# Performance work log

Hardware: AMD Instinct MI355X
Metric: run time of the kernel (lower is better)

Reference implementation:

```python
import jax, jax.numpy as jnp
import numpy as np

H_OUT = 8
W_OUT = 8
MAXG = 4  # max adaptive sampling grid per bin: ceil((H-1)/H_OUT) with H=32


def _flip_table():
    h, w = H_OUT, W_OUT
    ys = np.repeat(np.arange(h), w)
    xs = np.tile(np.arange(w), h)
    rys = np.repeat(np.arange(h - 1, -1, -1), w)
    # NOTE: original torch code does arange(w-1,-1,-1).reshape(h,1).repeat(1,w)
    # which makes reverse_xs a per-ROW reversal (requires h==w); replicated faithfully.
    rxs = np.repeat(np.arange(w - 1, -1, -1), w)
    i00 = ys * w + xs
    i01 = ys * w + rxs
    i10 = rys * w + xs
    i11 = rys * w + rxs
    # original stacks [i00, i01, i01, i10, i11]; idx_idxs in {0..3} so entry for
    # (y_rev=1,x_rev=0) is i01 (duplicated) and (1,1) hits i10; i11 is unused. Replicated.
    return jnp.asarray(np.stack([i00, i01, i01, i10, i11]), dtype=jnp.int32)

_TABLE = _flip_table()


def _axis_samples(start, bin_sz, grid, n_out, size):
    # start, bin_sz: [N] float; grid: [N] int (adaptive samples per bin along this axis)
    # returns low/high neighbor indices and corner weights, each [N, n_out*MAXG]
    N = start.shape[0]
    g_safe = jnp.maximum(grid, 1).astype(start.dtype)
    ph = jnp.arange(n_out, dtype=start.dtype)
    i = jnp.arange(MAXG, dtype=start.dtype)
    pos = (start[:, None, None]
           + ph[None, :, None] * bin_sz[:, None, None]
           + (i[None, None, :] + 0.5) * (bin_sz / g_safe)[:, None, None])  # [N,n_out,MAXG]
    valid = ((pos >= -1.0) & (pos <= size)
             & (jnp.arange(MAXG)[None, None, :] < grid[:, None, None]))
    p = jnp.clip(pos, 0.0, size - 1)
    low = jnp.floor(p).astype(jnp.int32)
    high = jnp.minimum(low + 1, size - 1)
    l = p - low.astype(p.dtype)
    vf = valid.astype(start.dtype)
    return (low.reshape(N, -1), high.reshape(N, -1),
            ((1.0 - l) * vf).reshape(N, -1), (l * vf).reshape(N, -1))


def _roi_align_flip(feats, batch_idxs, starts, goals):
    B, C, H, W = feats.shape
    N = starts.shape[0]
    s = starts.astype(feats.dtype)
    g = goals.astype(feats.dtype)
    y_min = jnp.minimum(s[:, 0], g[:, 0]); y_max = jnp.maximum(s[:, 0], g[:, 0])
    x_min = jnp.minimum(s[:, 1], g[:, 1]); x_max = jnp.maximum(s[:, 1], g[:, 1])
    y_rev = s[:, 0] > g[:, 0]
    x_rev = s[:, 1] > g[:, 1]
    # torchvision roi_align: aligned=True, spatial_scale=1.0, sampling_ratio=-1
    start_h = y_min - 0.5; start_w = x_min - 0.5
    roi_h = y_max - y_min; roi_w = x_max - x_min
    bin_h = roi_h / H_OUT; bin_w = roi_w / W_OUT
    gh = jnp.ceil(bin_h).astype(jnp.int32)
    gw = jnp.ceil(bin_w).astype(jnp.int32)
    count = jnp.maximum(gh * gw, 1).astype(feats.dtype)
    ylo, yhi, wy0, wy1 = _axis_samples(start_h, bin_h, gh, H_OUT, H)  # [N, H_OUT*MAXG]
    xlo, xhi, wx0, wx1 = _axis_samples(start_w, bin_w, gw, W_OUT, W)  # [N, W_OUT*MAXG]
    fv = feats.reshape(B, C, H * W)[batch_idxs]  # [N,C,H*W] per-box feature slab
    hM, wM = H_OUT * MAXG, W_OUT * MAXG

    def gath(yi, xi):
        lin = (yi[:, :, None] * W + xi[:, None, :]).reshape(N, 1, hM * wM)
        v = jnp.take_along_axis(fv, jnp.broadcast_to(lin, (N, C, hM * wM)), axis=2)
        return v.reshape(N, C, hM, wM)

    def outer(a, b):
        return a[:, None, :, None] * b[:, None, None, :]

    acc = (gath(ylo, xlo) * outer(wy0, wx0)
           + gath(ylo, xhi) * outer(wy0, wx1)
           + gath(yhi, xlo) * outer(wy1, wx0)
           + gath(yhi, xhi) * outer(wy1, wx1))  # [N,C,hM,wM]
    rois = acc.reshape(N, C, H_OUT, MAXG, W_OUT, MAXG).sum(axis=(3, 5))
    rois = rois / count[:, None, None, None]
    # per-box orientation flip via index-table gather
    idx_idxs = y_rev.astype(jnp.int32) * 2 + x_rev.astype(jnp.int32)
    sel = _TABLE[idx_idxs]  # [N, h*w]
    rflat = rois.reshape(N, C, H_OUT * W_OUT)
    out = jnp.take_along_axis(rflat, jnp.broadcast_to(sel[:, None, :], rflat.shape), axis=2)
    return out.reshape(N, C, H_OUT, W_OUT)


def setup_inputs() -> dict:
    key = jax.random.key(0)
    k1, k2, k3, k4 = jax.random.split(key, 4)
    B, C, H, W = 8, 64, 32, 32
    N = 1024  # B * A with A = 128 agents
    feats = jax.random.normal(k1, (B, C, H, W), dtype=jnp.float32)
    batch_idxs = jax.random.randint(k2, (N,), 0, B, dtype=jnp.int32)
    starts = jax.random.randint(k3, (N, 2), 0, H, dtype=jnp.int32)
    goals = jax.random.randint(k4, (N, 2), 0, H, dtype=jnp.int32)
    return {"feats": feats, "batch_idxs": batch_idxs, "starts": starts, "goals": goals}


def reference(feats, batch_idxs, starts, goals):
    return _roi_align_flip(feats, batch_idxs, starts, goals)
```

## Files before the change

### kernel.cpp

```cpp
#include <hip/hip_runtime.h>

#define H_OUT 8
#define W_OUT 8
#define MAXG 4
#define CCHUNK 8
#define RSLOTS 6

__global__ __launch_bounds__(256) void ordered_roi_kernel(
    const float* __restrict__ feats,
    const int*   __restrict__ batch_idxs,
    const int*   __restrict__ starts,
    const int*   __restrict__ goals,
    float*       __restrict__ out,
    int C, int CG)
{
    const int bx  = blockIdx.x;
    const int n   = bx / CG;
    const int cg  = bx - n * CG;
    const int tid = threadIdx.x;

    const float s0 = (float)starts[2 * n + 0];
    const float s1 = (float)starts[2 * n + 1];
    const float g0 = (float)goals[2 * n + 0];
    const float g1 = (float)goals[2 * n + 1];
    const float y_min = fminf(s0, g0), y_max = fmaxf(s0, g0);
    const float x_min = fminf(s1, g1), x_max = fmaxf(s1, g1);
    const bool  y_rev = s0 > g0;
    const bool  x_rev = s1 > g1;
    const float start_h = y_min - 0.5f;
    const float start_w = x_min - 0.5f;
    const float bin_h = (y_max - y_min) / (float)H_OUT;
    const float bin_w = (x_max - x_min) / (float)W_OUT;
    const int   gh = (int)ceilf(bin_h);
    const int   gw = (int)ceilf(bin_w);
    const float inv_count = 1.0f / fmaxf((float)(gh * gw), 1.0f);

    __shared__ int   s_rbase[2][H_OUT];
    __shared__ int   s_rcnt[2][H_OUT];
    __shared__ float s_rw[2][H_OUT][RSLOTS];
    __shared__ float s_t[CCHUNK][H_OUT][33];

    if (tid < 16) {
        const int axis = tid >> 3;
        const int ph   = tid & 7;
        const float start = axis ? start_w : start_h;
        const float bin   = axis ? bin_w  : bin_h;
        const int   grid  = axis ? gw     : gh;
        const float gsafe = (float)(grid > 1 ? grid : 1);
        float wloc[RSLOTS] = {0.f, 0.f, 0.f, 0.f, 0.f, 0.f};
        int base = 0, last = -1;
        for (int i = 0; i < grid && i < MAXG; ++i) {
            const float pos = start + (float)ph * bin + ((float)i + 0.5f) * (bin / gsafe);
            const float vf  = (pos >= -1.0f && pos <= 32.0f) ? 1.0f : 0.0f;
            const float p   = fminf(fmaxf(pos, 0.0f), 31.0f);
            const int   lo  = (int)floorf(p);
            const int   hi  = min(lo + 1, 31);
            const float l   = p - (float)lo;
            if (i == 0) base = lo;
            wloc[lo - base] += (1.0f - l) * vf;
            wloc[hi - base] += l * vf;
            last = hi;
        }
        s_rbase[axis][ph] = base;
        s_rcnt[axis][ph]  = (grid > 0) ? (last - base + 1) : 0;
        #pragma unroll
        for (int k = 0; k < RSLOTS; ++k) s_rw[axis][ph][k] = wloc[k];
    }
    __syncthreads();

    {
        const int cp = tid >> 6;
        const int py = (tid >> 3) & 7;
        const int xq = tid & 7;
        const int rb = s_rbase[0][py];
        const int rc = s_rcnt[0][py];

        const int b = batch_idxs[n];
        const float* __restrict__ fb =
            feats + ((size_t)b * C + (size_t)cg * CCHUNK) * 1024;
        const float* __restrict__ fc0 = fb + (size_t)cp * 1024 + xq * 4;
        const float* __restrict__ fc1 = fc0 + 4 * 1024;

        float a00 = 0.f, a01 = 0.f, a02 = 0.f, a03 = 0.f;
        float a10 = 0.f, a11 = 0.f, a12 = 0.f, a13 = 0.f;
        for (int j = 0; j < rc; ++j) {
            const float w = s_rw[0][py][j];
            const float4 r0 = *reinterpret_cast<const float4*>(fc0 + (rb + j) * 32);
            const float4 r1 = *reinterpret_cast<const float4*>(fc1 + (rb + j) * 32);
            a00 = fmaf(w, r0.x, a00); a01 = fmaf(w, r0.y, a01);
            a02 = fmaf(w, r0.z, a02); a03 = fmaf(w, r0.w, a03);
            a10 = fmaf(w, r1.x, a10); a11 = fmaf(w, r1.y, a11);
            a12 = fmaf(w, r1.z, a12); a13 = fmaf(w, r1.w, a13);
        }
        const int x0 = xq * 4;
        s_t[cp][py][x0 + 0] = a00; s_t[cp][py][x0 + 1] = a01;
        s_t[cp][py][x0 + 2] = a02; s_t[cp][py][x0 + 3] = a03;
        s_t[cp + 4][py][x0 + 0] = a10; s_t[cp + 4][py][x0 + 1] = a11;
        s_t[cp + 4][py][x0 + 2] = a12; s_t[cp + 4][py][x0 + 3] = a13;
    }
    __syncthreads();

    const int yx = tid & 63;
    const int y  = yx >> 3;
    const int xo = yx & 7;
    const int c0 = tid >> 6;

    int py, px;
    if (y_rev && x_rev)      { py = H_OUT - 1 - y; px = xo; }
    else if (y_rev || x_rev) { py = y;             px = W_OUT - 1 - y; }
    else                     { py = y;             px = xo; }

    const int xb = s_rbase[1][px];
    const int xc = s_rcnt[1][px];
    float acc0 = 0.0f, acc1 = 0.0f;
    for (int j = 0; j < xc; ++j) {
        const float w = s_rw[1][px][j];
        acc0 = fmaf(w, s_t[c0][py][xb + j],     acc0);
        acc1 = fmaf(w, s_t[c0 + 4][py][xb + j], acc1);
    }

    float* __restrict__ ob =
        out + ((size_t)n * C + (size_t)cg * CCHUNK) * (H_OUT * W_OUT);
    ob[tid]       = acc0 * inv_count;
    ob[tid + 256] = acc1 * inv_count;
}

extern "C" void kernel_launch(void* const* d_in, const int* in_sizes, int n_in,
                              void* d_out, int out_size, void* d_ws, size_t ws_size,
                              hipStream_t stream) {
    const float* feats      = (const float*)d_in[0];
    const int*   batch_idxs = (const int*)d_in[1];
    const int*   starts     = (const int*)d_in[2];
    const int*   goals      = (const int*)d_in[3];
    float*       out        = (float*)d_out;

    const int N  = in_sizes[1];
    const int C  = out_size / (N * H_OUT * W_OUT);
    const int CG = C / CCHUNK;

    ordered_roi_kernel<<<N * CG, 256, 0, stream>>>(feats, batch_idxs, starts, goals,
                                                   out, C, CG);
}
```

Baseline: 83.71 us.

## Precompute per-ROI interpolation tables in separate kernel, double channel chunk

Moves the per-box separable weight/base/count computation into a small preceding kernel that writes a table to workspace, so the main kernel reads weights from global memory instead of computing them per block with an extra barrier. Doubles the channel chunk per block to 16, halving the block count and amortising table reads, and uses float4 LDS stores with a padded row stride. This adds a second kernel launch and global table reads in exchange for removing redundant per-block setup work.

Measured after the change: 78.74 us. -5.9%, faster.

```diff
diff --git a/kernel.cpp b/kernel.cpp
--- a/kernel.cpp
+++ b/kernel.cpp
@@ -3,14 +3,71 @@
 #define H_OUT 8
 #define W_OUT 8
 #define MAXG 4
-#define CCHUNK 8
+#define CCHUNK 16
 #define RSLOTS 6
+#define TSTRIDE 160
 
-__global__ __launch_bounds__(256) void ordered_roi_kernel(
+__global__ __launch_bounds__(256) void build_tables(
+    const int* __restrict__ batch_idxs,
+    const int* __restrict__ starts,
+    const int* __restrict__ goals,
+    float*     __restrict__ tab, int N)
+{
+    const int t = blockIdx.x * 256 + threadIdx.x;
+    if (t >= N * 16) return;
+    const int n    = t >> 4;
+    const int slot = t & 15;
+    const int axis = slot >> 3;
+    const int ph   = slot & 7;
+
+    const float s0 = (float)starts[2 * n + 0];
+    const float s1 = (float)starts[2 * n + 1];
+    const float g0 = (float)goals[2 * n + 0];
+    const float g1 = (float)goals[2 * n + 1];
+    const float y_min = fminf(s0, g0), y_max = fmaxf(s0, g0);
+    const float x_min = fminf(s1, g1), x_max = fmaxf(s1, g1);
+    const float bin_h = (y_max - y_min) * 0.125f;
+    const float bin_w = (x_max - x_min) * 0.125f;
+    const int   gh = (int)ceilf(bin_h);
+    const int   gw = (int)ceilf(bin_w);
+
+    const float start = axis ? (x_min - 0.5f) : (y_min - 0.5f);
+    const float bin   = axis ? bin_w : bin_h;
+    const int   grid  = axis ? gw : gh;
+    const float gsafe = (float)(grid > 1 ? grid : 1);
+
+    float wloc[RSLOTS] = {0.f, 0.f, 0.f, 0.f, 0.f, 0.f};
+    int base = 0, last = -1;
+    for (int i = 0; i < grid; ++i) {
+        const float pos = start + (float)ph * bin + ((float)i + 0.5f) * (bin / gsafe);
+        const float vf  = (pos >= -1.0f && pos <= 32.0f) ? 1.0f : 0.0f;
+        const float p   = fminf(fmaxf(pos, 0.0f), 31.0f);
+        const int   lo  = (int)floorf(p);
+        const int   hi  = min(lo + 1, 31);
+        const float l   = p - (float)lo;
+        if (i == 0) base = lo;
+        wloc[lo - base] += (1.0f - l) * vf;
+        wloc[hi - base] += l * vf;
+        last = hi;
+    }
+
+    float* __restrict__ tb = tab + (size_t)n * TSTRIDE;
+    #pragma unroll
+    for (int k = 0; k < RSLOTS; ++k) tb[axis * 48 + ph * 6 + k] = wloc[k];
+    tb[96  + axis * 16 + ph] = (float)base;
+    tb[104 + axis * 16 + ph] = (float)((grid > 0) ? (last - base + 1) : 0);
+    if (slot == 0) {
+        const bool y_rev = s0 > g0;
+        const bool x_rev = s1 > g1;
+        tb[128] = 1.0f / fmaxf((float)(gh * gw), 1.0f);
+        tb[129] = (float)((y_rev ? 2 : 0) + (x_rev ? 1 : 0));
+        tb[130] = (float)batch_idxs[n];
+    }
+}
+
+__global__ __launch_bounds__(256) void roi_main(
     const float* __restrict__ feats,
-    const int*   __restrict__ batch_idxs,
-    const int*   __restrict__ starts,
-    const int*   __restrict__ goals,
+    const float* __restrict__ tab,
     float*       __restrict__ out,
     int C, int CG)
 {
@@ -19,84 +76,44 @@
     const int cg  = bx - n * CG;
     const int tid = threadIdx.x;
 
-    const float s0 = (float)starts[2 * n + 0];
-    const float s1 = (float)starts[2 * n + 1];
-    const float g0 = (float)goals[2 * n + 0];
-    const float g1 = (float)goals[2 * n + 1];
-    const float y_min = fminf(s0, g0), y_max = fmaxf(s0, g0);
-    const float x_min = fminf(s1, g1), x_max = fmaxf(s1, g1);
-    const bool  y_rev = s0 > g0;
-    const bool  x_rev = s1 > g1;
-    const float start_h = y_min - 0.5f;
-    const float start_w = x_min - 0.5f;
-    const float bin_h = (y_max - y_min) / (float)H_OUT;
-    const float bin_w = (x_max - x_min) / (float)W_OUT;
-    const int   gh = (int)ceilf(bin_h);
-    const int   gw = (int)ceilf(bin_w);
-    const float inv_count = 1.0f / fmaxf((float)(gh * gw), 1.0f);
+    const float* __restrict__ tb = tab + (size_t)n * TSTRIDE;
 
-    __shared__ int   s_rbase[2][H_OUT];
-    __shared__ int   s_rcnt[2][H_OUT];
-    __shared__ float s_rw[2][H_OUT][RSLOTS];
-    __shared__ float s_t[CCHUNK][H_OUT][33];
-
-    if (tid < 16) {
-        const int axis = tid >> 3;
-        const int ph   = tid & 7;
-        const float start = axis ? start_w : start_h;
-        const float bin   = axis ? bin_w  : bin_h;
-        const int   grid  = axis ? gw     : gh;
-        const float gsafe = (float)(grid > 1 ? grid : 1);
-        float wloc[RSLOTS] = {0.f, 0.f, 0.f, 0.f, 0.f, 0.f};
-        int base = 0, last = -1;
-        for (int i = 0; i < grid && i < MAXG; ++i) {
-            const float pos = start + (float)ph * bin + ((float)i + 0.5f) * (bin / gsafe);
-            const float vf  = (pos >= -1.0f && pos <= 32.0f) ? 1.0f : 0.0f;
-            const float p   = fminf(fmaxf(pos, 0.0f), 31.0f);
-            const int   lo  = (int)floorf(p);
-            const int   hi  = min(lo + 1, 31);
-            const float l   = p - (float)lo;
-            if (i == 0) base = lo;
-            wloc[lo - base] += (1.0f - l) * vf;
-            wloc[hi - base] += l * vf;
-            last = hi;
-        }
-        s_rbase[axis][ph] = base;
-        s_rcnt[axis][ph]  = (grid > 0) ? (last - base + 1) : 0;
-        #pragma unroll
-        for (int k = 0; k < RSLOTS; ++k) s_rw[axis][ph][k] = wloc[k];
-    }
-    __syncthreads();
+    __shared__ float s_t[CCHUNK][H_OUT][36];
 
     {
         const int cp = tid >> 6;
         const int py = (tid >> 3) & 7;
         const int xq = tid & 7;
-        const int rb = s_rbase[0][py];
-        const int rc = s_rcnt[0][py];
+        const int rb = (int)tb[96 + py];
+        const int rc = (int)tb[104 + py];
+        const int b  = (int)tb[130];
 
-        const int b = batch_idxs[n];
         const float* __restrict__ fb =
-            feats + ((size_t)b * C + (size_t)cg * CCHUNK) * 1024;
-        const float* __restrict__ fc0 = fb + (size_t)cp * 1024 + xq * 4;
-        const float* __restrict__ fc1 = fc0 + 4 * 1024;
+            feats + ((size_t)b * C + (size_t)(cg * CCHUNK + cp * 4)) * 1024 + xq * 4;
 
-        float a00 = 0.f, a01 = 0.f, a02 = 0.f, a03 = 0.f;
-        float a10 = 0.f, a11 = 0.f, a12 = 0.f, a13 = 0.f;
+        float4 a0 = {0.f,0.f,0.f,0.f}, a1 = {0.f,0.f,0.f,0.f};
+        float4 a2 = {0.f,0.f,0.f,0.f}, a3 = {0.f,0.f,0.f,0.f};
         for (int j = 0; j < rc; ++j) {
-            const float w = s_rw[0][py][j];
-            const float4 r0 = *reinterpret_cast<const float4*>(fc0 + (rb + j) * 32);
-            const float4 r1 = *reinterpret_cast<const float4*>(fc1 + (rb + j) * 32);
-            a00 = fmaf(w, r0.x, a00); a01 = fmaf(w, r0.y, a01);
-            a02 = fmaf(w, r0.z, a02); a03 = fmaf(w, r0.w, a03);
-            a10 = fmaf(w, r1.x, a10); a11 = fmaf(w, r1.y, a11);
-            a12 = fmaf(w, r1.z, a12); a13 = fmaf(w, r1.w, a13);
+            const float w  = tb[py * 6 + j];
+            const int   ro = (rb + j) * 32;
+            const float4 r0 = *reinterpret_cast<const float4*>(fb + ro);
+            const float4 r1 = *reinterpret_cast<const float4*>(fb + 1024 + ro);
+            const float4 r2 = *reinterpret_cast<const float4*>(fb + 2048 + ro);
+            const float4 r3 = *reinterpret_cast<const float4*>(fb + 3072 + ro);
+            a0.x = fmaf(w, r0.x, a0.x); a0.y = fmaf(w, r0.y, a0.y);
+            a0.z = fmaf(w, r0.z, a0.z); a0.w = fmaf(w, r0.w, a0.w);
+            a1.x = fmaf(w, r1.x, a1.x); a1.y = fmaf(w, r1.y, a1.y);
+            a1.z = fmaf(w, r1.z, a1.z); a1.w = fmaf(w, r1.w, a1.w);
+            a2.x = fmaf(w, r2.x, a2.x); a2.y = fmaf(w, r2.y, a2.y);
+            a2.z = fmaf(w, r2.z, a2.z); a2.w = fmaf(w, r2.w, a2.w);
+            a3.x = fmaf(w, r3.x, a3.x); a3.y = fmaf(w, r3.y, a3.y);
+            a3.z = fmaf(w, r3.z, a3.z); a3.w = fmaf(w, r3.w, a3.w);
         }
         const int x0 = xq * 4;
-        s_t[cp][py][x0 + 0] = a00; s_t[cp][py][x0 + 1] = a01;
-        s_t[cp][py][x0 + 2] = a02; s_t[cp][py][x0 + 3] = a03;
-        s_t[cp + 4][py][x0 + 0] = a10; s_t[cp + 4][py][x0 + 1] = a11;
-        s_t[cp + 4][py][x0 + 2] = a12; s_t[cp + 4][py][x0 + 3] = a13;
+        *reinterpret_cast<float4*>(&s_t[cp * 4 + 0][py][x0]) = a0;
+        *reinterpret_cast<float4*>(&s_t[cp * 4 + 1][py][x0]) = a1;
+        *reinterpret_cast<float4*>(&s_t[cp * 4 + 2][py][x0]) = a2;
+        *reinterpret_cast<float4*>(&s_t[cp * 4 + 3][py][x0]) = a3;
     }
     __syncthreads();
 
@@ -105,24 +122,31 @@
     const int xo = yx & 7;
     const int c0 = tid >> 6;
 
+    const int fc = (int)tb[129];
     int py, px;
-    if (y_rev && x_rev)      { py = H_OUT - 1 - y; px = xo; }
-    else if (y_rev || x_rev) { py = y;             px = W_OUT - 1 - y; }
-    else                     { py = y;             px = xo; }
+    if (fc == 3)      { py = H_OUT - 1 - y; px = xo; }
+    else if (fc != 0) { py = y;             px = W_OUT - 1 - y; }
+    else              { py = y;             px = xo; }
 
-    const int xb = s_rbase[1][px];
-    const int xc = s_rcnt[1][px];
-    float acc0 = 0.0f, acc1 = 0.0f;
+    const int   xb = (int)tb[112 + px];
+    const int   xc = (int)tb[120 + px];
+    const float inv_count = tb[128];
+
+    float b0 = 0.f, b1 = 0.f, b2 = 0.f, b3 = 0.f;
     for (int j = 0; j < xc; ++j) {
-        const float w = s_rw[1][px][j];
-        acc0 = fmaf(w, s_t[c0][py][xb + j],     acc0);
-        acc1 = fmaf(w, s_t[c0 + 4][py][xb + j], acc1);
+        const float w = tb[48 + px * 6 + j];
+        b0 = fmaf(w, s_t[c0     ][py][xb + j], b0);
+        b1 = fmaf(w, s_t[c0 +  4][py][xb + j], b1);
+        b2 = fmaf(w, s_t[c0 +  8][py][xb + j], b2);
+        b3 = fmaf(w, s_t[c0 + 12][py][xb + j], b3);
     }
 
     float* __restrict__ ob =
         out + ((size_t)n * C + (size_t)cg * CCHUNK) * (H_OUT * W_OUT);
-    ob[tid]       = acc0 * inv_count;
-    ob[tid + 256] = acc1 * inv_count;
+    ob[tid      ] = b0 * inv_count;
+    ob[tid + 256] = b1 * inv_count;
+    ob[tid + 512] = b2 * inv_count;
+    ob[tid + 768] = b3 * inv_count;
 }
 
 extern "C" void kernel_launch(void* const* d_in, const int* in_sizes, int n_in,
@@ -133,11 +157,13 @@
     const int*   starts     = (const int*)d_in[2];
     const int*   goals      = (const int*)d_in[3];
     float*       out        = (float*)d_out;
+    float*       tab        = (float*)d_ws;
 
     const int N  = in_sizes[1];
     const int C  = out_size / (N * H_OUT * W_OUT);
     const int CG = C / CCHUNK;
 
-    ordered_roi_kernel<<<N * CG, 256, 0, stream>>>(feats, batch_idxs, starts, goals,
-                                                   out, C, CG);
+    const int tb_blocks = (N * 16 + 255) / 256;
+    build_tables<<<tb_blocks, 256, 0, stream>>>(batch_idxs, starts, goals, tab, N);
+    roi_main<<<N * CG, 256, 0, stream>>>(feats, tab, out, C, CG);
 }
```
